# Kernel optimization log

Measured on AMD Instinct MI355X. Metric: run time of the kernel, lower is better.

The kernel has to match this reference:

```python
import jax, jax.numpy as jnp
import numpy as np

T, B, OBS, H, A = 512, 64, 512, 1024, 18


def setup_inputs() -> dict:
    key = jax.random.key(0)
    ks = jax.random.split(key, 8)
    s = lambda fan: 1.0 / np.sqrt(fan)
    return {
        "obs": jax.random.normal(ks[0], (T, B, OBS), jnp.float32),
        # binary done/valid mask per (timestep, env)
        "mask": (jax.random.uniform(ks[1], (T, B)) > 0.05).astype(jnp.float32),
        "W_enc": jax.random.normal(ks[2], (H, OBS), jnp.float32) * s(OBS),
        "b_enc": jnp.zeros((H,), jnp.float32),
        "W_ih": jax.random.normal(ks[3], (4 * H, H), jnp.float32) * s(H),
        "b_ih": jnp.zeros((4 * H,), jnp.float32),
        "W_hh": jax.random.normal(ks[4], (4 * H, H), jnp.float32) * s(H),
        "b_hh": jnp.zeros((4 * H,), jnp.float32),
        "W_dec": jax.random.normal(ks[5], (A, H), jnp.float32) * s(H),
        "b_dec": jnp.zeros((A,), jnp.float32),
    }


def reference(obs, mask, W_enc, b_enc, W_ih, b_ih, W_hh, b_hh, W_dec, b_dec):
    # encoder MLP + relu, batched over all T*B (one big GEMM)
    encoded = jax.nn.relu(jnp.einsum("tbo,ho->tbh", obs, W_enc) + b_enc)
    # precompute input contribution to LSTM gates for all timesteps: [T,B,4H]
    x_gates = jnp.einsum("tbh,gh->tbg", encoded, W_ih) + b_ih + b_hh

    def step(carry, inp):
        h, c = carry
        xg, m = inp  # xg: [B,4H], m: [B]
        gates = xg + h @ W_hh.T
        i, f, g, o = jnp.split(gates, 4, axis=-1)  # torch LSTMCell order
        c_new = jax.nn.sigmoid(f) * c + jax.nn.sigmoid(i) * jnp.tanh(g)
        h_new = jax.nn.sigmoid(o) * jnp.tanh(c_new)
        m = m[:, None]
        h_new = h_new * m
        c_new = c_new * m
        return (h_new, c_new), h_new

    h0 = jnp.zeros((B, H), jnp.float32)
    c0 = jnp.zeros((B, H), jnp.float32)
    (h, c), latent = jax.lax.scan(step, (h0, c0), (x_gates, mask))

    # decoder over flattened (T*B, H) then mask q-values
    values = jnp.einsum("tbh,ah->tba", latent, W_dec) + b_dec
    values = values * mask[..., None]
    return values, h, c
```

## Files before the change

kernel.cpp:

```cpp
#include <hip/hip_runtime.h>
#include <hip/hip_bf16.h>

#define T_ 512
#define B_ 64
#define OBS_ 512
#define H_ 1024
#define A_ 18
#define MM_ (T_*B_)
#define G4_ (4*H_)
#define CH_ 64
#define NCH_ (T_/CH_)
#define CM_ (CH_*B_)

typedef unsigned short u16;
typedef __attribute__((ext_vector_type(8))) short s8v;
typedef __attribute__((ext_vector_type(4))) float f4v;

__device__ __forceinline__ float b2f(u16 u){
    unsigned x = ((unsigned)u) << 16;
    return __builtin_bit_cast(float, x);
}
__device__ __forceinline__ u16 f2b(float f){
    unsigned x = __builtin_bit_cast(unsigned, f);
    return (u16)((x + 0x7fffu + ((x >> 16) & 1u)) >> 16);
}


__global__ void cast_f32_bf16(const float* __restrict__ in, u16* __restrict__ out, int n){
    int i = blockIdx.x * blockDim.x + threadIdx.x;
    int stride = gridDim.x * blockDim.x;
    for (; i < n; i += stride) out[i] = f2b(in[i]);
}

__global__ void add_bias2(const float* __restrict__ a, const float* __restrict__ b,
                          float* __restrict__ out, int n){
    int i = blockIdx.x * blockDim.x + threadIdx.x;
    if (i < n) out[i] = a[i] + b[i];
}

__global__ void zero_init(u16* __restrict__ h0, float* __restrict__ c,
                          unsigned* __restrict__ cnt, int n){
    int i = blockIdx.x * blockDim.x + threadIdx.x;
    if (i < n){ h0[i] = 0; c[i] = 0.f; }
    if (i < 256) cnt[i] = 0u;
}

__global__ void copy_hc(const float* __restrict__ h, const float* __restrict__ c,
                        float* __restrict__ out){
    int i = blockIdx.x * blockDim.x + threadIdx.x;
    out[(size_t)MM_*A_ + i] = h[i];
    out[(size_t)MM_*A_ + B_*H_ + i] = c[i];
}


#define LDSS 72

template<bool A_FP32, bool RELU>
__global__ __launch_bounds__(256) void gemm_bt(
    const void* __restrict__ Aptr, const u16* __restrict__ W,
    const float* __restrict__ bias, u16* __restrict__ C,
    int M, int N, int K)
{
    __shared__ __align__(16) u16 As[128 * LDSS];
    __shared__ __align__(16) u16 Bs[128 * LDSS];

    const int tid  = threadIdx.x;
    const int lane = tid & 63;
    const int wid  = tid >> 6;
    const int wm   = wid & 1, wn = wid >> 1;
    const int m0   = blockIdx.y * 128, n0 = blockIdx.x * 128;
    const int quad = lane >> 4, l16 = lane & 15;

    f4v acc[4][4];
    #pragma unroll
    for (int i = 0; i < 4; i++)
        #pragma unroll
        for (int j = 0; j < 4; j++) acc[i][j] = (f4v){0.f,0.f,0.f,0.f};

    for (int k0 = 0; k0 < K; k0 += 64){
        __syncthreads();
        if (A_FP32){
            const float* A = (const float*)Aptr;
            #pragma unroll
            for (int pss = 0; pss < 8; pss++){
                int idx = pss * 256 + tid;
                int row = idx >> 4, ch = idx & 15;
                float4 v = *(const float4*)(A + (size_t)(m0 + row) * K + k0 + ch * 4);
                u16* d = &As[row * LDSS + ch * 4];
                d[0] = f2b(v.x); d[1] = f2b(v.y); d[2] = f2b(v.z); d[3] = f2b(v.w);
            }
        } else {
            const u16* A = (const u16*)Aptr;
            #pragma unroll
            for (int pss = 0; pss < 4; pss++){
                int idx = pss * 256 + tid;
                int row = idx >> 3, ch = idx & 7;
                *(uint4*)&As[row * LDSS + ch * 8] =
                    *(const uint4*)(A + (size_t)(m0 + row) * K + k0 + ch * 8);
            }
        }
        #pragma unroll
        for (int pss = 0; pss < 4; pss++){
            int idx = pss * 256 + tid;
            int row = idx >> 3, ch = idx & 7;
            *(uint4*)&Bs[row * LDSS + ch * 8] =
                *(const uint4*)(W + (size_t)(n0 + row) * K + k0 + ch * 8);
        }
        __syncthreads();

        #pragma unroll
        for (int kk = 0; kk < 64; kk += 32){
            s8v af[4], bf[4];
            #pragma unroll
            for (int mt = 0; mt < 4; mt++)
                af[mt] = *(const s8v*)&As[(wm*64 + mt*16 + l16) * LDSS + kk + quad*8];
            #pragma unroll
            for (int nt = 0; nt < 4; nt++)
                bf[nt] = *(const s8v*)&Bs[(wn*64 + nt*16 + l16) * LDSS + kk + quad*8];
            #pragma unroll
            for (int mt = 0; mt < 4; mt++)
                #pragma unroll
                for (int nt = 0; nt < 4; nt++)
                    acc[mt][nt] = __builtin_amdgcn_mfma_f32_16x16x32_bf16(
                        af[mt], bf[nt], acc[mt][nt], 0, 0, 0);
        }
    }

    #pragma unroll
    for (int mt = 0; mt < 4; mt++){
        #pragma unroll
        for (int nt = 0; nt < 4; nt++){
            #pragma unroll
            for (int r = 0; r < 4; r++){
                int m = m0 + wm*64 + mt*16 + quad*4 + r;
                int n = n0 + wn*64 + nt*16 + l16;
                float v = acc[mt][nt][r] + bias[n];
                if (RELU) v = fmaxf(v, 0.f);
                C[(size_t)m * N + n] = f2b(v);
            }
        }
    }
}


__global__ __launch_bounds__(256, 2) void lstm_scan(
    const u16* __restrict__ xg,
    const u16* __restrict__ Whh,
    u16* __restrict__ h_hist,
    float* __restrict__ c_glob,
    float* __restrict__ h_f32,
    const float* __restrict__ mask,
    unsigned* __restrict__ cnt,
    int t0)
{
    __shared__ float red[4][4][16][16];

    const int tid  = threadIdx.x;
    const int lane = tid & 63;
    const int w    = tid >> 6;
    const int quad = lane >> 4, l16 = lane & 15;
    const int bid  = blockIdx.x;
    const int g = (bid & 7) >> 1;
    const int s = ((bid >> 3) << 1) | (bid & 1);
    const int rb0 = g * 16, j0 = s * 16;
    unsigned* mycnt = cnt + (g << 6);

    const int koff = w * 256;
    s8v bf[4][8];
    #pragma unroll
    for (int gate = 0; gate < 4; gate++)
        #pragma unroll
        for (int ks = 0; ks < 8; ks++)
            bf[gate][ks] = *(const s8v*)(
                Whh + (size_t)(gate * H_ + j0 + l16) * H_ + koff + ks * 32 + quad * 8);

    const int cb = tid >> 4, cu = tid & 15;
    const size_t cidx = (size_t)(rb0 + cb) * H_ + j0 + cu;
    float c_reg = c_glob[cidx];

    for (int st = 0; st < CH_; st++){
        const u16* hs = h_hist + (size_t)st * B_ * H_;

        f4v acc[4];
        #pragma unroll
        for (int gate = 0; gate < 4; gate++) acc[gate] = (f4v){0.f,0.f,0.f,0.f};
        #pragma unroll
        for (int ks = 0; ks < 8; ks++){
            s8v af = *(const s8v*)(hs + (size_t)(rb0 + l16) * H_ + koff + ks * 32 + quad * 8);
            #pragma unroll
            for (int gate = 0; gate < 4; gate++)
                acc[gate] = __builtin_amdgcn_mfma_f32_16x16x32_bf16(af, bf[gate][ks], acc[gate], 0, 0, 0);
        }
        #pragma unroll
        for (int gate = 0; gate < 4; gate++)
            #pragma unroll
            for (int r = 0; r < 4; r++)
                red[w][gate][quad * 4 + r][l16] = acc[gate][r];
        __syncthreads();

        const u16* xgt = xg + (size_t)st * B_ * G4_ + (size_t)(rb0 + cb) * G4_ + j0 + cu;
        float gi = 0.f, gf = 0.f, gg = 0.f, go = 0.f;
        #pragma unroll
        for (int ww = 0; ww < 4; ww++){
            gi += red[ww][0][cb][cu];
            gf += red[ww][1][cb][cu];
            gg += red[ww][2][cb][cu];
            go += red[ww][3][cb][cu];
        }
        gi += b2f(xgt[0]);
        gf += b2f(xgt[H_]);
        gg += b2f(xgt[2 * H_]);
        go += b2f(xgt[3 * H_]);

        float is = 1.f / (1.f + __expf(-gi));
        float fs = 1.f / (1.f + __expf(-gf));
        float os = 1.f / (1.f + __expf(-go));
        float gt = tanhf(gg);

        float cn = fs * c_reg + is * gt;
        float hn = os * tanhf(cn);
        float m  = mask[(size_t)st * B_ + rb0 + cb];
        hn *= m; cn *= m;
        c_reg = cn;
        if (t0 + st == T_ - 1) h_f32[cidx] = hn;

        unsigned hb = (unsigned)f2b(hn);
        unsigned partner = (unsigned)__shfl_xor((int)hb, 1, 64);
        if ((cu & 1) == 0){
            unsigned packed = hb | (partner << 16);
            unsigned* dst = (unsigned*)(h_hist + (size_t)(st + 1) * B_ * H_ + cidx);
            __hip_atomic_store(dst, packed, __ATOMIC_RELAXED, __HIP_MEMORY_SCOPE_AGENT);
            if (st == CH_ - 1){
                unsigned* dst0 = (unsigned*)(h_hist + cidx);
                __hip_atomic_store(dst0, packed, __ATOMIC_RELAXED, __HIP_MEMORY_SCOPE_AGENT);
            }
        }
        asm volatile("s_waitcnt vmcnt(0)" ::: "memory");
        __syncthreads();

        if (tid == 0){
            __hip_atomic_fetch_add(mycnt, 1u, __ATOMIC_RELAXED, __HIP_MEMORY_SCOPE_AGENT);
            if (st < CH_ - 1){
                const unsigned target = (unsigned)(t0 + st + 1) * 64u;
                while (__hip_atomic_load(mycnt, __ATOMIC_RELAXED, __HIP_MEMORY_SCOPE_AGENT) < target)
                    __builtin_amdgcn_s_sleep(4);
            }
        }
        __syncthreads();
    }

    c_glob[cidx] = c_reg;
}


__global__ __launch_bounds__(256) void decode_kernel(
    const u16* __restrict__ latent, const u16* __restrict__ Wdec,
    const float* __restrict__ bdec, const float* __restrict__ mask,
    float* __restrict__ values, int rows)
{
    __shared__ __align__(16) u16 wl[A_ * H_];
    const int tid = threadIdx.x;
    for (int i = tid; i < A_ * H_ / 8; i += 256)
        ((uint4*)wl)[i] = ((const uint4*)Wdec)[i];
    __syncthreads();

    const int lane = tid & 63;
    int wid = blockIdx.x * 4 + (tid >> 6);
    const int nwaves = gridDim.x * 4;

    for (int row = wid; row < rows; row += nwaves){
        float lat[16];
        #pragma unroll
        for (int i = 0; i < 16; i++)
            lat[i] = b2f(latent[(size_t)row * H_ + i*64 + lane]);
        float acc[A_];
        #pragma unroll
        for (int a = 0; a < A_; a++) acc[a] = 0.f;
        #pragma unroll
        for (int i = 0; i < 16; i++){
            #pragma unroll
            for (int a = 0; a < A_; a++)
                acc[a] += lat[i] * b2f(wl[a * H_ + i*64 + lane]);
        }
        float m = mask[row];
        #pragma unroll
        for (int a = 0; a < A_; a++){
            float v = acc[a];
            #pragma unroll
            for (int s = 32; s > 0; s >>= 1) v += __shfl_down(v, s, 64);
            if (lane == 0) values[(size_t)row * A_ + a] = (v + bdec[a]) * m;
        }
    }
}


extern "C" void kernel_launch(void* const* d_in, const int* in_sizes, int n_in,
                              void* d_out, int out_size, void* d_ws, size_t ws_size,
                              hipStream_t stream)
{
    const float* obs  = (const float*)d_in[0];
    const float* mask = (const float*)d_in[1];
    const float* Wenc = (const float*)d_in[2];
    const float* benc = (const float*)d_in[3];
    const float* Wih  = (const float*)d_in[4];
    const float* bih  = (const float*)d_in[5];
    const float* Whh  = (const float*)d_in[6];
    const float* bhh  = (const float*)d_in[7];
    const float* Wdec = (const float*)d_in[8];
    const float* bdec = (const float*)d_in[9];
    float* out = (float*)d_out;

    char* p = (char*)d_ws;
    size_t o = 0;
    auto alloc = [&](size_t bytes){ void* r = p + o; o += (bytes + 255) & ~(size_t)255; return r; };
    u16*      wenc_b  = (u16*)     alloc((size_t)H_ * OBS_ * 2);
    u16*      wih_b   = (u16*)     alloc((size_t)G4_ * H_ * 2);
    u16*      whh_b   = (u16*)     alloc((size_t)G4_ * H_ * 2);
    u16*      wdec_b  = (u16*)     alloc((size_t)A_ * H_ * 2);
    float*    bias2   = (float*)   alloc((size_t)G4_ * 4);
    u16*      enc_ch  = (u16*)     alloc((size_t)CM_ * H_ * 2);
    u16*      xg_ch   = (u16*)     alloc((size_t)CM_ * G4_ * 2);
    u16*      h_hist  = (u16*)     alloc((size_t)(CH_ + 1) * B_ * H_ * 2);
    float*    h_f32   = (float*)   alloc((size_t)B_ * H_ * 4);
    float*    c_f32   = (float*)   alloc((size_t)B_ * H_ * 4);
    unsigned* cnt     = (unsigned*)alloc(256 * 4);
    (void)ws_size; (void)in_sizes; (void)n_in; (void)out_size;

    cast_f32_bf16<<<1024, 256, 0, stream>>>(Wenc, wenc_b, H_ * OBS_);
    cast_f32_bf16<<<2048, 256, 0, stream>>>(Wih,  wih_b,  G4_ * H_);
    cast_f32_bf16<<<2048, 256, 0, stream>>>(Whh,  whh_b,  G4_ * H_);
    cast_f32_bf16<<<72,   256, 0, stream>>>(Wdec, wdec_b, A_ * H_);
    add_bias2<<<16, 256, 0, stream>>>(bih, bhh, bias2, G4_);
    zero_init<<<256, 256, 0, stream>>>(h_hist, c_f32, cnt, B_ * H_);

    for (int c = 0; c < NCH_; c++){
        const int t0 = c * CH_;

        dim3 g1(H_ / 128, CM_ / 128);
        gemm_bt<true, true><<<g1, 256, 0, stream>>>(
            obs + (size_t)t0 * B_ * OBS_, wenc_b, benc, enc_ch, CM_, H_, OBS_);

        dim3 g2(G4_ / 128, CM_ / 128);
        gemm_bt<false, false><<<g2, 256, 0, stream>>>(
            enc_ch, wih_b, bias2, xg_ch, CM_, G4_, H_);

        lstm_scan<<<256, 256, 0, stream>>>(
            xg_ch, whh_b, h_hist, c_f32, h_f32,
            mask + (size_t)t0 * B_, cnt, t0);

        decode_kernel<<<256, 256, 0, stream>>>(
            h_hist + (size_t)B_ * H_, wdec_b, bdec, mask + (size_t)t0 * B_,
            out + (size_t)t0 * B_ * A_, CM_);
    }

    copy_hc<<<256, 256, 0, stream>>>(h_f32, c_f32, out);
}
```

Baseline: 2.885 ms.

## Replace LSTM step counter barrier with NaN-sentinel polling on hidden-state history

The per-step atomic counter barrier in the recurrent scan is removed. Instead, each h_hist slot is prefilled with a bf16 NaN pattern, and each block spins on its own A-operand loads until none of the words are NaN. The decoder writes the sentinel back into each slot once it has consumed that row, so the buffer is ready for the next chunk. The aim is to cut the global barrier round trip and the extra block syncs from the serial step, while the xg and mask loads are moved ahead of the wait so they overlap it. The costs are extra sentinel-fill traffic, a correctness dependence on no real hidden value matching the NaN pattern, and a bounded spin with a silent fallback if the wait times out.

```diff
diff --git a/kernel.cpp b/kernel.cpp
--- a/kernel.cpp
+++ b/kernel.cpp
@@ -13,8 +13,13 @@
 #define CM_ (CH_*B_)
 
 typedef unsigned short u16;
+typedef unsigned long long u64;
 typedef __attribute__((ext_vector_type(8))) short s8v;
 typedef __attribute__((ext_vector_type(4))) float f4v;
+typedef __attribute__((ext_vector_type(2))) u64 u64x2;
+
+#define NAN16_PAT 0x7FC07FC07FC07FC0ULL
+#define NAN32_PAT 0x7FC07FC0u
 
 __device__ __forceinline__ float b2f(u16 u){
     unsigned x = ((unsigned)u) << 16;
@@ -23,6 +28,10 @@
 __device__ __forceinline__ u16 f2b(float f){
     unsigned x = __builtin_bit_cast(unsigned, f);
     return (u16)((x + 0x7fffu + ((x >> 16) & 1u)) >> 16);
+}
+__device__ __forceinline__ u64 nan16(u64 x){
+    u64 y = x ^ NAN16_PAT;
+    return (y - 0x0001000100010001ULL) & ~y & 0x8000800080008000ULL;
 }
 
 
@@ -38,11 +47,14 @@
     if (i < n) out[i] = a[i] + b[i];
 }
 
-__global__ void zero_init(u16* __restrict__ h0, float* __restrict__ c,
-                          unsigned* __restrict__ cnt, int n){
+__global__ void init_scan(u16* __restrict__ h_hist, float* __restrict__ c){
     int i = blockIdx.x * blockDim.x + threadIdx.x;
-    if (i < n){ h0[i] = 0; c[i] = 0.f; }
-    if (i < 256) cnt[i] = 0u;
+    int stride = gridDim.x * blockDim.x;
+    unsigned* h0 = (unsigned*)h_hist;
+    for (int k = i; k < B_*H_/2; k += stride) h0[k] = 0u;
+    for (int k = i; k < B_*H_; k += stride) c[k] = 0.f;
+    unsigned* p = (unsigned*)(h_hist + (size_t)B_*H_);
+    for (int k = i; k < CH_*B_*H_/2; k += stride) p[k] = NAN32_PAT;
 }
 
 __global__ void copy_hc(const float* __restrict__ h, const float* __restrict__ c,
@@ -143,14 +155,13 @@
 }
 
 
-__global__ __launch_bounds__(256, 2) void lstm_scan(
+__global__ __launch_bounds__(256, 1) void lstm_scan(
     const u16* __restrict__ xg,
     const u16* __restrict__ Whh,
     u16* __restrict__ h_hist,
     float* __restrict__ c_glob,
     float* __restrict__ h_f32,
     const float* __restrict__ mask,
-    unsigned* __restrict__ cnt,
     int t0)
 {
     __shared__ float red[4][4][16][16];
@@ -160,10 +171,9 @@
     const int w    = tid >> 6;
     const int quad = lane >> 4, l16 = lane & 15;
     const int bid  = blockIdx.x;
-    const int g = (bid & 7) >> 1;
-    const int s = ((bid >> 3) << 1) | (bid & 1);
+    const int g = bid & 3;
+    const int s = bid >> 2;
     const int rb0 = g * 16, j0 = s * 16;
-    unsigned* mycnt = cnt + (g << 6);
 
     const int koff = w * 256;
     s8v bf[4][8];
@@ -178,15 +188,39 @@
     const size_t cidx = (size_t)(rb0 + cb) * H_ + j0 + cu;
     float c_reg = c_glob[cidx];
 
+    const size_t hoff = (size_t)(rb0 + l16) * H_ + koff + quad * 8;
+
     for (int st = 0; st < CH_; st++){
-        const u16* hs = h_hist + (size_t)st * B_ * H_;
+        const u16* xgt = xg + (size_t)st * B_ * G4_ + (size_t)(rb0 + cb) * G4_ + j0 + cu;
+        float xi = b2f(xgt[0]);
+        float xf = b2f(xgt[H_]);
+        float xv = b2f(xgt[2 * H_]);
+        float xo = b2f(xgt[3 * H_]);
+        float m  = mask[(size_t)st * B_ + rb0 + cb];
+
+        const u64* hp = (const u64*)(h_hist + (size_t)st * B_ * H_ + hoff);
+        u64 v[16];
+        int tries = 0;
+        for (;;){
+            #pragma unroll
+            for (int ks = 0; ks < 8; ks++){
+                v[2*ks]   = __hip_atomic_load(hp + ks*8,     __ATOMIC_RELAXED, __HIP_MEMORY_SCOPE_AGENT);
+                v[2*ks+1] = __hip_atomic_load(hp + ks*8 + 1, __ATOMIC_RELAXED, __HIP_MEMORY_SCOPE_AGENT);
+            }
+            u64 bad = 0;
+            #pragma unroll
+            for (int i = 0; i < 16; i++) bad |= nan16(v[i]);
+            if (!__any(bad != 0)) break;
+            if (++tries > (1 << 22)) break;
+        }
 
         f4v acc[4];
         #pragma unroll
         for (int gate = 0; gate < 4; gate++) acc[gate] = (f4v){0.f,0.f,0.f,0.f};
         #pragma unroll
         for (int ks = 0; ks < 8; ks++){
-            s8v af = *(const s8v*)(hs + (size_t)(rb0 + l16) * H_ + koff + ks * 32 + quad * 8);
+            u64x2 t = { v[2*ks], v[2*ks+1] };
+            s8v af = __builtin_bit_cast(s8v, t);
             #pragma unroll
             for (int gate = 0; gate < 4; gate++)
                 acc[gate] = __builtin_amdgcn_mfma_f32_16x16x32_bf16(af, bf[gate][ks], acc[gate], 0, 0, 0);
@@ -198,8 +232,7 @@
                 red[w][gate][quad * 4 + r][l16] = acc[gate][r];
         __syncthreads();
 
-        const u16* xgt = xg + (size_t)st * B_ * G4_ + (size_t)(rb0 + cb) * G4_ + j0 + cu;
-        float gi = 0.f, gf = 0.f, gg = 0.f, go = 0.f;
+        float gi = xi, gf = xf, gg = xv, go = xo;
         #pragma unroll
         for (int ww = 0; ww < 4; ww++){
             gi += red[ww][0][cb][cu];
@@ -207,10 +240,6 @@
             gg += red[ww][2][cb][cu];
             go += red[ww][3][cb][cu];
         }
-        gi += b2f(xgt[0]);
-        gf += b2f(xgt[H_]);
-        gg += b2f(xgt[2 * H_]);
-        go += b2f(xgt[3 * H_]);
 
         float is = 1.f / (1.f + __expf(-gi));
         float fs = 1.f / (1.f + __expf(-gf));
@@ -219,7 +248,6 @@
 
         float cn = fs * c_reg + is * gt;
         float hn = os * tanhf(cn);
-        float m  = mask[(size_t)st * B_ + rb0 + cb];
         hn *= m; cn *= m;
         c_reg = cn;
         if (t0 + st == T_ - 1) h_f32[cidx] = hn;
@@ -235,18 +263,7 @@
                 __hip_atomic_store(dst0, packed, __ATOMIC_RELAXED, __HIP_MEMORY_SCOPE_AGENT);
             }
         }
-        asm volatile("s_waitcnt vmcnt(0)" ::: "memory");
         __syncthreads();
-
-        if (tid == 0){
-            __hip_atomic_fetch_add(mycnt, 1u, __ATOMIC_RELAXED, __HIP_MEMORY_SCOPE_AGENT);
-            if (st < CH_ - 1){
-                const unsigned target = (unsigned)(t0 + st + 1) * 64u;
-                while (__hip_atomic_load(mycnt, __ATOMIC_RELAXED, __HIP_MEMORY_SCOPE_AGENT) < target)
-                    __builtin_amdgcn_s_sleep(4);
-            }
-        }
-        __syncthreads();
     }
 
     c_glob[cidx] = c_reg;
@@ -254,7 +271,7 @@
 
 
 __global__ __launch_bounds__(256) void decode_kernel(
-    const u16* __restrict__ latent, const u16* __restrict__ Wdec,
+    u16* __restrict__ latent, const u16* __restrict__ Wdec,
     const float* __restrict__ bdec, const float* __restrict__ mask,
     float* __restrict__ values, int rows)
 {
@@ -290,6 +307,9 @@
             for (int s = 32; s > 0; s >>= 1) v += __shfl_down(v, s, 64);
             if (lane == 0) values[(size_t)row * A_ + a] = (v + bdec[a]) * m;
         }
+        unsigned* lrow = (unsigned*)(latent + (size_t)row * H_);
+        #pragma unroll
+        for (int i = 0; i < 8; i++) lrow[lane + i*64] = NAN32_PAT;
     }
 }
 
@@ -323,7 +343,6 @@
     u16*      h_hist  = (u16*)     alloc((size_t)(CH_ + 1) * B_ * H_ * 2);
     float*    h_f32   = (float*)   alloc((size_t)B_ * H_ * 4);
     float*    c_f32   = (float*)   alloc((size_t)B_ * H_ * 4);
-    unsigned* cnt     = (unsigned*)alloc(256 * 4);
     (void)ws_size; (void)in_sizes; (void)n_in; (void)out_size;
 
     cast_f32_bf16<<<1024, 256, 0, stream>>>(Wenc, wenc_b, H_ * OBS_);
@@ -331,7 +350,7 @@
     cast_f32_bf16<<<2048, 256, 0, stream>>>(Whh,  whh_b,  G4_ * H_);
     cast_f32_bf16<<<72,   256, 0, stream>>>(Wdec, wdec_b, A_ * H_);
     add_bias2<<<16, 256, 0, stream>>>(bih, bhh, bias2, G4_);
-    zero_init<<<256, 256, 0, stream>>>(h_hist, c_f32, cnt, B_ * H_);
+    init_scan<<<2048, 256, 0, stream>>>(h_hist, c_f32);
 
     for (int c = 0; c < NCH_; c++){
         const int t0 = c * CH_;
@@ -346,7 +365,7 @@
 
         lstm_scan<<<256, 256, 0, stream>>>(
             xg_ch, whh_b, h_hist, c_f32, h_f32,
-            mask + (size_t)t0 * B_, cnt, t0);
+            mask + (size_t)t0 * B_, t0);
 
         decode_kernel<<<256, 256, 0, stream>>>(
             h_hist + (size_t)B_ * H_, wdec_b, bdec, mask + (size_t)t0 * B_,
```

After: 3.441 ms. 19.3% more time.

## Replace counter barrier with per-block flags polled by all lanes; prefetch xg and mask

Applied to the files above, without the earlier changes.

The per-step group barrier changes from a single atomic counter incremented by every block (polled by thread 0 with sleeps) to per-block progress flags. Each lane polls a few flags with 64-bit loads until all 64 producers in the batch group reach the step. The next step's xg gates and mask are prefetched after publishing h so their latency is hidden, and the LDS reduction buffer is padded to avoid bank conflicts. The spin loop has a bailout cap after which it proceeds without the dependency, and the block-to-group mapping is changed.

```diff
diff --git a/kernel.cpp b/kernel.cpp
--- a/kernel.cpp
+++ b/kernel.cpp
@@ -13,6 +13,7 @@
 #define CM_ (CH_*B_)
 
 typedef unsigned short u16;
+typedef unsigned long long u64;
 typedef __attribute__((ext_vector_type(8))) short s8v;
 typedef __attribute__((ext_vector_type(4))) float f4v;
 
@@ -38,11 +39,14 @@
     if (i < n) out[i] = a[i] + b[i];
 }
 
-__global__ void zero_init(u16* __restrict__ h0, float* __restrict__ c,
-                          unsigned* __restrict__ cnt, int n){
+__global__ void init_scan(u16* __restrict__ h_hist, float* __restrict__ c,
+                          unsigned* __restrict__ flags){
     int i = blockIdx.x * blockDim.x + threadIdx.x;
-    if (i < n){ h0[i] = 0; c[i] = 0.f; }
-    if (i < 256) cnt[i] = 0u;
+    int stride = gridDim.x * blockDim.x;
+    unsigned* h0 = (unsigned*)h_hist;
+    for (int k = i; k < B_*H_/2; k += stride) h0[k] = 0u;
+    for (int k = i; k < B_*H_; k += stride) c[k] = 0.f;
+    if (i < 256) flags[i] = 0u;
 }
 
 __global__ void copy_hc(const float* __restrict__ h, const float* __restrict__ c,
@@ -143,27 +147,25 @@
 }
 
 
-__global__ __launch_bounds__(256, 2) void lstm_scan(
+__global__ __launch_bounds__(256, 1) void lstm_scan(
     const u16* __restrict__ xg,
     const u16* __restrict__ Whh,
     u16* __restrict__ h_hist,
     float* __restrict__ c_glob,
     float* __restrict__ h_f32,
     const float* __restrict__ mask,
-    unsigned* __restrict__ cnt,
+    unsigned* __restrict__ flags,
     int t0)
 {
-    __shared__ float red[4][4][16][16];
+    __shared__ float red[4][4][16][17];
 
     const int tid  = threadIdx.x;
     const int lane = tid & 63;
     const int w    = tid >> 6;
     const int quad = lane >> 4, l16 = lane & 15;
     const int bid  = blockIdx.x;
-    const int g = (bid & 7) >> 1;
-    const int s = ((bid >> 3) << 1) | (bid & 1);
+    const int g = bid & 3, s = bid >> 2;
     const int rb0 = g * 16, j0 = s * 16;
-    unsigned* mycnt = cnt + (g << 6);
 
     const int koff = w * 256;
     s8v bf[4][8];
@@ -178,15 +180,36 @@
     const size_t cidx = (size_t)(rb0 + cb) * H_ + j0 + cu;
     float c_reg = c_glob[cidx];
 
+    const size_t hoff = (size_t)(rb0 + l16) * H_ + koff + quad * 8;
+    unsigned* gflags = flags + (g << 6);
+    const u64* fp = (const u64*)gflags + ((lane & 15) << 1);
+
+    const u16* xg0 = xg + (size_t)(rb0 + cb) * G4_ + j0 + cu;
+    u16 nxi = xg0[0], nxf = xg0[H_], nxv = xg0[2 * H_], nxo = xg0[3 * H_];
+    float nm = mask[rb0 + cb];
+
     for (int st = 0; st < CH_; st++){
-        const u16* hs = h_hist + (size_t)st * B_ * H_;
-
+        const float xi = b2f(nxi), xf = b2f(nxf), xv = b2f(nxv), xo = b2f(nxo);
+        const float m = nm;
+
+        const unsigned tgt = (unsigned)(t0 + st);
+        int tries = 0;
+        for (;;){
+            u64 f0 = __hip_atomic_load(fp,     __ATOMIC_RELAXED, __HIP_MEMORY_SCOPE_AGENT);
+            u64 f1 = __hip_atomic_load(fp + 1, __ATOMIC_RELAXED, __HIP_MEMORY_SCOPE_AGENT);
+            bool ok = ((unsigned)f0 >= tgt) & ((unsigned)(f0 >> 32) >= tgt)
+                    & ((unsigned)f1 >= tgt) & ((unsigned)(f1 >> 32) >= tgt);
+            if (__all(ok)) break;
+            if (++tries > (1 << 20)) break;
+        }
+
+        const u16* hs = h_hist + (size_t)st * B_ * H_ + hoff;
         f4v acc[4];
         #pragma unroll
         for (int gate = 0; gate < 4; gate++) acc[gate] = (f4v){0.f,0.f,0.f,0.f};
         #pragma unroll
         for (int ks = 0; ks < 8; ks++){
-            s8v af = *(const s8v*)(hs + (size_t)(rb0 + l16) * H_ + koff + ks * 32 + quad * 8);
+            s8v af = *(const s8v*)(hs + ks * 32);
             #pragma unroll
             for (int gate = 0; gate < 4; gate++)
                 acc[gate] = __builtin_amdgcn_mfma_f32_16x16x32_bf16(af, bf[gate][ks], acc[gate], 0, 0, 0);
@@ -198,8 +221,7 @@
                 red[w][gate][quad * 4 + r][l16] = acc[gate][r];
         __syncthreads();
 
-        const u16* xgt = xg + (size_t)st * B_ * G4_ + (size_t)(rb0 + cb) * G4_ + j0 + cu;
-        float gi = 0.f, gf = 0.f, gg = 0.f, go = 0.f;
+        float gi = xi, gf = xf, gg = xv, go = xo;
         #pragma unroll
         for (int ww = 0; ww < 4; ww++){
             gi += red[ww][0][cb][cu];
@@ -207,10 +229,6 @@
             gg += red[ww][2][cb][cu];
             go += red[ww][3][cb][cu];
         }
-        gi += b2f(xgt[0]);
-        gf += b2f(xgt[H_]);
-        gg += b2f(xgt[2 * H_]);
-        go += b2f(xgt[3 * H_]);
 
         float is = 1.f / (1.f + __expf(-gi));
         float fs = 1.f / (1.f + __expf(-gf));
@@ -219,7 +237,6 @@
 
         float cn = fs * c_reg + is * gt;
         float hn = os * tanhf(cn);
-        float m  = mask[(size_t)st * B_ + rb0 + cb];
         hn *= m; cn *= m;
         c_reg = cn;
         if (t0 + st == T_ - 1) h_f32[cidx] = hn;
@@ -238,15 +255,15 @@
         asm volatile("s_waitcnt vmcnt(0)" ::: "memory");
         __syncthreads();
 
-        if (tid == 0){
-            __hip_atomic_fetch_add(mycnt, 1u, __ATOMIC_RELAXED, __HIP_MEMORY_SCOPE_AGENT);
-            if (st < CH_ - 1){
-                const unsigned target = (unsigned)(t0 + st + 1) * 64u;
-                while (__hip_atomic_load(mycnt, __ATOMIC_RELAXED, __HIP_MEMORY_SCOPE_AGENT) < target)
-                    __builtin_amdgcn_s_sleep(4);
-            }
-        }
-        __syncthreads();
+        if (tid == 0)
+            __hip_atomic_store(gflags + s, (unsigned)(t0 + st + 1),
+                               __ATOMIC_RELAXED, __HIP_MEMORY_SCOPE_AGENT);
+
+        if (st + 1 < CH_){
+            const u16* xgn = xg + (size_t)(st + 1) * B_ * G4_ + (size_t)(rb0 + cb) * G4_ + j0 + cu;
+            nxi = xgn[0]; nxf = xgn[H_]; nxv = xgn[2 * H_]; nxo = xgn[3 * H_];
+            nm = mask[(size_t)(st + 1) * B_ + rb0 + cb];
+        }
     }
 
     c_glob[cidx] = c_reg;
@@ -323,7 +340,7 @@
     u16*      h_hist  = (u16*)     alloc((size_t)(CH_ + 1) * B_ * H_ * 2);
     float*    h_f32   = (float*)   alloc((size_t)B_ * H_ * 4);
     float*    c_f32   = (float*)   alloc((size_t)B_ * H_ * 4);
-    unsigned* cnt     = (unsigned*)alloc(256 * 4);
+    unsigned* flags   = (unsigned*)alloc(256 * 4);
     (void)ws_size; (void)in_sizes; (void)n_in; (void)out_size;
 
     cast_f32_bf16<<<1024, 256, 0, stream>>>(Wenc, wenc_b, H_ * OBS_);
@@ -331,7 +348,7 @@
     cast_f32_bf16<<<2048, 256, 0, stream>>>(Whh,  whh_b,  G4_ * H_);
     cast_f32_bf16<<<72,   256, 0, stream>>>(Wdec, wdec_b, A_ * H_);
     add_bias2<<<16, 256, 0, stream>>>(bih, bhh, bias2, G4_);
-    zero_init<<<256, 256, 0, stream>>>(h_hist, c_f32, cnt, B_ * H_);
+    init_scan<<<2048, 256, 0, stream>>>(h_hist, c_f32, flags);
 
     for (int c = 0; c < NCH_; c++){
         const int t0 = c * CH_;
@@ -346,7 +363,7 @@
 
         lstm_scan<<<256, 256, 0, stream>>>(
             xg_ch, whh_b, h_hist, c_f32, h_f32,
-            mask + (size_t)t0 * B_, cnt, t0);
+            mask + (size_t)t0 * B_, flags, t0);
 
         decode_kernel<<<256, 256, 0, stream>>>(
             h_hist + (size_t)B_ * H_, wdec_b, bdec, mask + (size_t)t0 * B_,
```

New measurement: 2.757 ms. 4.4% less time.
